# Performance work log

Measured on AMD Instinct MI355X. Metric: run time of the kernel, lower is better.

The kernel has to match this reference:

```python
import jax, jax.numpy as jnp
import numpy as np

SIZE = 7
SIGMA = 1.5
K1 = 0.01
K2 = 0.03
DATA_RANGE = 2.0
NP_ = SIZE * SIZE
COV_NORM = NP_ / (NP_ - 1)
PAD = SIZE // 2


def _gaussian_window(size=SIZE, sigma=SIGMA, channels=1):
    x = np.arange(size) - size // 2
    g = np.exp(-x**2 / (2.0 * sigma**2))[None, :]
    g = (g.T @ g)
    g = g / g.sum()
    w = np.tile(g[None, None], (channels, 1, 1, 1))  # [C,1,size,size]
    return jnp.asarray(w, dtype=jnp.float32)


def _dwconv(x, w):
    # depthwise conv2d, zero padding PAD, stride 1; x: [N,C,H,W], w: [C,1,k,k]
    c = x.shape[1]
    return jax.lax.conv_general_dilated(
        x, w, window_strides=(1, 1), padding=[(PAD, PAD), (PAD, PAD)],
        dimension_numbers=('NCHW', 'OIHW', 'NCHW'), feature_group_count=c)


def setup_inputs() -> dict:
    key = jax.random.key(0)
    k1, k2 = jax.random.split(key)
    X = jax.random.uniform(k1, (64, 1, 320, 320), dtype=jnp.float32)
    Y = jax.random.uniform(k2, (64, 1, 320, 320), dtype=jnp.float32)
    window = _gaussian_window()
    return {"X": X, "Y": Y, "window": window}


def reference(X, Y, window):
    C1 = (K1 * DATA_RANGE) ** 2
    C2 = (K2 * DATA_RANGE) ** 2
    mux = _dwconv(X, window)
    muy = _dwconv(Y, window)
    mux_sq = mux * mux
    muy_sq = muy * muy
    muxy = mux * muy
    sigmax_sq = (_dwconv(X * X, window) - mux_sq) * COV_NORM
    sigmay_sq = (_dwconv(Y * Y, window) - muy_sq) * COV_NORM
    sigmaxy = (_dwconv(X * Y, window) - muxy) * COV_NORM
    ssim_map = ((2 * muxy + C1) * (2 * sigmaxy + C2)) / \
               ((mux_sq + muy_sq + C1) * (sigmax_sq + sigmay_sq + C2))
    return 1.0 - ssim_map.mean()
```

## Files before the change

### kernel.cpp

```cpp
#include <hip/hip_runtime.h>
#include <math.h>


#define TW 64
#define TH 16
#define LW 72
#define LH 22
#define WI 320
#define HI 320
#define NI 64
#define NBLK (5 * 20 * NI)
#define NPIX ((double)NI * WI * HI)

typedef float v4 __attribute__((ext_vector_type(4)));

struct W7 { float w[7]; };

__global__ __launch_bounds__(256) void ssim_kernel(
    const float* __restrict__ X, const float* __restrict__ Y,
    W7 wv, float* __restrict__ partial)
{
    __shared__ __align__(16) float buf[5 * LH * 64];
    __shared__ float wsum[4];

    float* sX = buf;
    float* sY = buf + LH * LW;

    const int tid = threadIdx.x;
    const int tx0 = blockIdx.x * TW;
    const int ty0 = blockIdx.y * TH;
    const int n   = blockIdx.z;
    const float* __restrict__ Xn = X + (size_t)n * (WI * HI);
    const float* __restrict__ Yn = Y + (size_t)n * (WI * HI);

    for (int i = tid; i < LH * LW; i += 256) {
        int r  = i / LW;
        int c  = i - r * LW;
        int gy = ty0 - 3 + r;
        int gx = tx0 - 3 + c;
        float xv = 0.f, yv = 0.f;
        if (c < 70 && (unsigned)gy < (unsigned)HI && (unsigned)gx < (unsigned)WI) {
            int idx = gy * WI + gx;
            xv = Xn[idx];
            yv = Yn[idx];
        }
        sX[i] = xv;
        sY[i] = yv;
    }
    __syncthreads();

    float hreg[2][5][4];
#pragma unroll
    for (int it = 0; it < 2; ++it) {
        int g = tid + it * 256;
        if (g < 352) {
            int r  = g >> 4;
            int c0 = (g & 15) << 2;
            const v4* px = (const v4*)&sX[r * LW + c0];
            const v4* py = (const v4*)&sY[r * LW + c0];
            v4 xa = px[0], xb = px[1], xc = px[2];
            v4 ya = py[0], yb = py[1], yc = py[2];
            float xv[12] = {xa.x,xa.y,xa.z,xa.w, xb.x,xb.y,xb.z,xb.w, xc.x,xc.y,xc.z,xc.w};
            float yv[12] = {ya.x,ya.y,ya.z,ya.w, yb.x,yb.y,yb.z,yb.w, yc.x,yc.y,yc.z,yc.w};
            float xx[12], yy[12], xy[12];
#pragma unroll
            for (int e = 0; e < 12; ++e) {
                xx[e] = xv[e] * xv[e];
                yy[e] = yv[e] * yv[e];
                xy[e] = xv[e] * yv[e];
            }
#pragma unroll
            for (int j = 0; j < 4; ++j) {
                float ax = 0.f, ay = 0.f, axx = 0.f, ayy = 0.f, axy = 0.f;
#pragma unroll
                for (int d = 0; d < 7; ++d) {
                    float w = wv.w[d];
                    ax  += w * xv[j + d];
                    ay  += w * yv[j + d];
                    axx += w * xx[j + d];
                    ayy += w * yy[j + d];
                    axy += w * xy[j + d];
                }
                hreg[it][0][j] = ax;  hreg[it][1][j] = ay;
                hreg[it][2][j] = axx; hreg[it][3][j] = ayy; hreg[it][4][j] = axy;
            }
        }
    }
    __syncthreads();

#pragma unroll
    for (int it = 0; it < 2; ++it) {
        int g = tid + it * 256;
        if (g < 352) {
            int r  = g >> 4;
            int c0 = (g & 15) << 2;
#pragma unroll
            for (int ch = 0; ch < 5; ++ch) {
                v4 t = { hreg[it][ch][0], hreg[it][ch][1],
                         hreg[it][ch][2], hreg[it][ch][3] };
                *(v4*)&buf[ch * (LH * 64) + r * 64 + c0] = t;
            }
        }
    }
    __syncthreads();

    {
        int r  = tid >> 4;
        int c0 = (tid & 15) << 2;
        v4 mx  = {0.f,0.f,0.f,0.f}, my  = {0.f,0.f,0.f,0.f};
        v4 sxx = {0.f,0.f,0.f,0.f}, syy = {0.f,0.f,0.f,0.f}, sxy = {0.f,0.f,0.f,0.f};
#pragma unroll
        for (int d = 0; d < 7; ++d) {
            float w = wv.w[d];
            int off = (r + d) * 64 + c0;
            mx  += w * *(const v4*)&buf[0 * 1408 + off];
            my  += w * *(const v4*)&buf[1 * 1408 + off];
            sxx += w * *(const v4*)&buf[2 * 1408 + off];
            syy += w * *(const v4*)&buf[3 * 1408 + off];
            sxy += w * *(const v4*)&buf[4 * 1408 + off];
        }
        const float C1 = 0.0004f, C2 = 0.0036f, COVN = 49.f / 48.f;
        v4 mxsq = mx * mx;
        v4 mysq = my * my;
        v4 mxy  = mx * my;
        v4 vx   = (sxx - mxsq) * COVN;
        v4 vy   = (syy - mysq) * COVN;
        v4 vxy  = (sxy - mxy)  * COVN;
        v4 num  = (2.f * mxy + C1) * (2.f * vxy + C2);
        v4 den  = (mxsq + mysq + C1) * (vx + vy + C2);
        v4 q;
        q.x = num.x * __builtin_amdgcn_rcpf(den.x);
        q.y = num.y * __builtin_amdgcn_rcpf(den.y);
        q.z = num.z * __builtin_amdgcn_rcpf(den.z);
        q.w = num.w * __builtin_amdgcn_rcpf(den.w);
        float lsum = (q.x + q.y) + (q.z + q.w);

#pragma unroll
        for (int off = 32; off > 0; off >>= 1)
            lsum += __shfl_down(lsum, off, 64);
        if ((tid & 63) == 0) wsum[tid >> 6] = lsum;
        __syncthreads();
        if (tid == 0) {
            int bid = (blockIdx.z * gridDim.y + blockIdx.y) * gridDim.x + blockIdx.x;
            partial[bid] = (wsum[0] + wsum[1]) + (wsum[2] + wsum[3]);
        }
    }
}

__global__ __launch_bounds__(256) void ssim_finalize(
    const float* __restrict__ partial, float* __restrict__ out)
{
    __shared__ double ws[4];
    const int tid = threadIdx.x;
    double s = 0.0;
    for (int i = tid; i < NBLK; i += 256) s += (double)partial[i];
#pragma unroll
    for (int off = 32; off > 0; off >>= 1)
        s += __shfl_down(s, off, 64);
    if ((tid & 63) == 0) ws[tid >> 6] = s;
    __syncthreads();
    if (tid == 0)
        out[0] = (float)(1.0 - ((ws[0] + ws[1]) + (ws[2] + ws[3])) / NPIX);
}

extern "C" void kernel_launch(void* const* d_in, const int* in_sizes, int n_in,
                              void* d_out, int out_size, void* d_ws, size_t ws_size,
                              hipStream_t stream) {
    const float* X = (const float*)d_in[0];
    const float* Y = (const float*)d_in[1];
    W7 wv;
    {
        double g[7], s = 0.0;
        for (int i = 0; i < 7; ++i) {
            double x = (double)(i - 3);
            g[i] = exp(-(x * x) / (2.0 * 1.5 * 1.5));
            s += g[i];
        }
        for (int i = 0; i < 7; ++i) wv.w[i] = (float)(g[i] / s);
    }

    float* partial = (float*)d_ws;

    dim3 grid(WI / TW, HI / TH, NI);
    ssim_kernel<<<grid, 256, 0, stream>>>(X, Y, wv, partial);
    ssim_finalize<<<1, 256, 0, stream>>>(partial, (float*)d_out);
}
```

Measured before the change: 122.1 us.

## Reorder separable SSIM to vertical-first column tasks reading global directly

```diff
diff --git a/kernel.cpp b/kernel.cpp
--- a/kernel.cpp
+++ b/kernel.cpp
@@ -2,148 +2,139 @@
 #include <math.h>
 
 
-#define TW 64
-#define TH 16
-#define LW 72
-#define LH 22
 #define WI 320
 #define HI 320
 #define NI 64
-#define NBLK (5 * 20 * NI)
+#define TW 64
+#define TH 32
+#define GXD 5
+#define GYD 10
+#define NBLK (GXD * GYD * NI)
+#define LSTR 72
 #define NPIX ((double)NI * WI * HI)
 
 typedef float v4 __attribute__((ext_vector_type(4)));
 
 struct W7 { float w[7]; };
 
+template <bool INTERIOR>
+__device__ __forceinline__ void column_task(
+    const float* __restrict__ Xn, const float* __restrict__ Yn,
+    const W7& wv, float* __restrict__ vbuf, int tx0, int ty0, int band, int ci)
+{
+    const int gx  = tx0 + ci - 3;
+    const bool xok = (unsigned)gx < (unsigned)WI;
+    const int gy0 = ty0 + band * 8 - 3;
+
+    float acc[5][8];
+#pragma unroll
+    for (int ch = 0; ch < 5; ++ch)
+#pragma unroll
+        for (int r = 0; r < 8; ++r) acc[ch][r] = 0.f;
+
+#pragma unroll
+    for (int j = 0; j < 14; ++j) {
+        const int gy = gy0 + j;
+        float xv = 0.f, yv = 0.f;
+        const bool ok = INTERIOR ? xok : (xok && ((unsigned)gy < (unsigned)HI));
+        if (ok) {
+            int idx = gy * WI + gx;
+            xv = Xn[idx];
+            yv = Yn[idx];
+        }
+        const float pxx = xv * xv, pyy = yv * yv, pxy = xv * yv;
+#pragma unroll
+        for (int r = 0; r < 8; ++r) {
+            const int d = j - r;
+            if (d >= 0 && d < 7) {
+                const float w = wv.w[d];
+                acc[0][r] += w * xv;
+                acc[1][r] += w * yv;
+                acc[2][r] += w * pxx;
+                acc[3][r] += w * pyy;
+                acc[4][r] += w * pxy;
+            }
+        }
+    }
+#pragma unroll
+    for (int ch = 0; ch < 5; ++ch)
+#pragma unroll
+        for (int r = 0; r < 8; ++r)
+            vbuf[ch * (TH * LSTR) + (band * 8 + r) * LSTR + (ci + 1)] = acc[ch][r];
+}
+
 __global__ __launch_bounds__(256) void ssim_kernel(
     const float* __restrict__ X, const float* __restrict__ Y,
     W7 wv, float* __restrict__ partial)
 {
-    __shared__ __align__(16) float buf[5 * LH * 64];
+    __shared__ __align__(16) float vbuf[5 * TH * LSTR];
     __shared__ float wsum[4];
-
-    float* sX = buf;
-    float* sY = buf + LH * LW;
 
     const int tid = threadIdx.x;
     const int tx0 = blockIdx.x * TW;
     const int ty0 = blockIdx.y * TH;
-    const int n   = blockIdx.z;
-    const float* __restrict__ Xn = X + (size_t)n * (WI * HI);
-    const float* __restrict__ Yn = Y + (size_t)n * (WI * HI);
+    const float* __restrict__ Xn = X + (size_t)blockIdx.z * (WI * HI);
+    const float* __restrict__ Yn = Y + (size_t)blockIdx.z * (WI * HI);
 
-    for (int i = tid; i < LH * LW; i += 256) {
-        int r  = i / LW;
-        int c  = i - r * LW;
-        int gy = ty0 - 3 + r;
-        int gx = tx0 - 3 + c;
-        float xv = 0.f, yv = 0.f;
-        if (c < 70 && (unsigned)gy < (unsigned)HI && (unsigned)gx < (unsigned)WI) {
-            int idx = gy * WI + gx;
-            xv = Xn[idx];
-            yv = Yn[idx];
-        }
-        sX[i] = xv;
-        sY[i] = yv;
+    const bool interior = (blockIdx.y >= 1) && (blockIdx.y <= GYD - 2);
+    if (interior) {
+        column_task<true>(Xn, Yn, wv, vbuf, tx0, ty0, tid >> 6, tid & 63);
+        if (tid < 24) column_task<true>(Xn, Yn, wv, vbuf, tx0, ty0, tid / 6, 64 + tid % 6);
+    } else {
+        column_task<false>(Xn, Yn, wv, vbuf, tx0, ty0, tid >> 6, tid & 63);
+        if (tid < 24) column_task<false>(Xn, Yn, wv, vbuf, tx0, ty0, tid / 6, 64 + tid % 6);
     }
     __syncthreads();
 
-    float hreg[2][5][4];
+    const float C1 = 0.0004f, C2 = 0.0036f, COVN = 49.f / 48.f;
+    const int xg   = (tid & 15) << 2;
+    const int row0 = tid >> 4;
+
+    float lsum = 0.f;
 #pragma unroll
-    for (int it = 0; it < 2; ++it) {
-        int g = tid + it * 256;
-        if (g < 352) {
-            int r  = g >> 4;
-            int c0 = (g & 15) << 2;
-            const v4* px = (const v4*)&sX[r * LW + c0];
-            const v4* py = (const v4*)&sY[r * LW + c0];
-            v4 xa = px[0], xb = px[1], xc = px[2];
-            v4 ya = py[0], yb = py[1], yc = py[2];
-            float xv[12] = {xa.x,xa.y,xa.z,xa.w, xb.x,xb.y,xb.z,xb.w, xc.x,xc.y,xc.z,xc.w};
-            float yv[12] = {ya.x,ya.y,ya.z,ya.w, yb.x,yb.y,yb.z,yb.w, yc.x,yc.y,yc.z,yc.w};
-            float xx[12], yy[12], xy[12];
+    for (int pass = 0; pass < 2; ++pass) {
+        const int row = row0 + pass * 16;
+        float f[5][12];
 #pragma unroll
-            for (int e = 0; e < 12; ++e) {
-                xx[e] = xv[e] * xv[e];
-                yy[e] = yv[e] * yv[e];
-                xy[e] = xv[e] * yv[e];
+        for (int ch = 0; ch < 5; ++ch) {
+            const v4* p = (const v4*)&vbuf[ch * (TH * LSTR) + row * LSTR + xg];
+            v4 a = p[0], b = p[1], c = p[2];
+            f[ch][0] = a.x; f[ch][1] = a.y; f[ch][2]  = a.z; f[ch][3]  = a.w;
+            f[ch][4] = b.x; f[ch][5] = b.y; f[ch][6]  = b.z; f[ch][7]  = b.w;
+            f[ch][8] = c.x; f[ch][9] = c.y; f[ch][10] = c.z; f[ch][11] = c.w;
+        }
+#pragma unroll
+        for (int j = 0; j < 4; ++j) {
+            float mx = 0.f, my = 0.f, sxx = 0.f, syy = 0.f, sxy = 0.f;
+#pragma unroll
+            for (int d = 0; d < 7; ++d) {
+                const float w = wv.w[d];
+                mx  += w * f[0][j + d + 1];
+                my  += w * f[1][j + d + 1];
+                sxx += w * f[2][j + d + 1];
+                syy += w * f[3][j + d + 1];
+                sxy += w * f[4][j + d + 1];
             }
-#pragma unroll
-            for (int j = 0; j < 4; ++j) {
-                float ax = 0.f, ay = 0.f, axx = 0.f, ayy = 0.f, axy = 0.f;
-#pragma unroll
-                for (int d = 0; d < 7; ++d) {
-                    float w = wv.w[d];
-                    ax  += w * xv[j + d];
-                    ay  += w * yv[j + d];
-                    axx += w * xx[j + d];
-                    ayy += w * yy[j + d];
-                    axy += w * xy[j + d];
-                }
-                hreg[it][0][j] = ax;  hreg[it][1][j] = ay;
-                hreg[it][2][j] = axx; hreg[it][3][j] = ayy; hreg[it][4][j] = axy;
-            }
+            const float mxsq = mx * mx;
+            const float mysq = my * my;
+            const float mxy  = mx * my;
+            const float vx   = (sxx - mxsq) * COVN;
+            const float vy   = (syy - mysq) * COVN;
+            const float vxy  = (sxy - mxy)  * COVN;
+            const float num  = (2.f * mxy + C1) * (2.f * vxy + C2);
+            const float den  = (mxsq + mysq + C1) * (vx + vy + C2);
+            lsum += num * __builtin_amdgcn_rcpf(den);
         }
     }
-    __syncthreads();
 
 #pragma unroll
-    for (int it = 0; it < 2; ++it) {
-        int g = tid + it * 256;
-        if (g < 352) {
-            int r  = g >> 4;
-            int c0 = (g & 15) << 2;
-#pragma unroll
-            for (int ch = 0; ch < 5; ++ch) {
-                v4 t = { hreg[it][ch][0], hreg[it][ch][1],
-                         hreg[it][ch][2], hreg[it][ch][3] };
-                *(v4*)&buf[ch * (LH * 64) + r * 64 + c0] = t;
-            }
-        }
-    }
+    for (int off = 32; off > 0; off >>= 1)
+        lsum += __shfl_down(lsum, off, 64);
+    if ((tid & 63) == 0) wsum[tid >> 6] = lsum;
     __syncthreads();
-
-    {
-        int r  = tid >> 4;
-        int c0 = (tid & 15) << 2;
-        v4 mx  = {0.f,0.f,0.f,0.f}, my  = {0.f,0.f,0.f,0.f};
-        v4 sxx = {0.f,0.f,0.f,0.f}, syy = {0.f,0.f,0.f,0.f}, sxy = {0.f,0.f,0.f,0.f};
-#pragma unroll
-        for (int d = 0; d < 7; ++d) {
-            float w = wv.w[d];
-            int off = (r + d) * 64 + c0;
-            mx  += w * *(const v4*)&buf[0 * 1408 + off];
-            my  += w * *(const v4*)&buf[1 * 1408 + off];
-            sxx += w * *(const v4*)&buf[2 * 1408 + off];
-            syy += w * *(const v4*)&buf[3 * 1408 + off];
-            sxy += w * *(const v4*)&buf[4 * 1408 + off];
-        }
-        const float C1 = 0.0004f, C2 = 0.0036f, COVN = 49.f / 48.f;
-        v4 mxsq = mx * mx;
-        v4 mysq = my * my;
-        v4 mxy  = mx * my;
-        v4 vx   = (sxx - mxsq) * COVN;
-        v4 vy   = (syy - mysq) * COVN;
-        v4 vxy  = (sxy - mxy)  * COVN;
-        v4 num  = (2.f * mxy + C1) * (2.f * vxy + C2);
-        v4 den  = (mxsq + mysq + C1) * (vx + vy + C2);
-        v4 q;
-        q.x = num.x * __builtin_amdgcn_rcpf(den.x);
-        q.y = num.y * __builtin_amdgcn_rcpf(den.y);
-        q.z = num.z * __builtin_amdgcn_rcpf(den.z);
-        q.w = num.w * __builtin_amdgcn_rcpf(den.w);
-        float lsum = (q.x + q.y) + (q.z + q.w);
-
-#pragma unroll
-        for (int off = 32; off > 0; off >>= 1)
-            lsum += __shfl_down(lsum, off, 64);
-        if ((tid & 63) == 0) wsum[tid >> 6] = lsum;
-        __syncthreads();
-        if (tid == 0) {
-            int bid = (blockIdx.z * gridDim.y + blockIdx.y) * gridDim.x + blockIdx.x;
-            partial[bid] = (wsum[0] + wsum[1]) + (wsum[2] + wsum[3]);
-        }
+    if (tid == 0) {
+        int bid = (blockIdx.z * GYD + blockIdx.y) * GXD + blockIdx.x;
+        partial[bid] = (wsum[0] + wsum[1]) + (wsum[2] + wsum[3]);
     }
 }
 
@@ -181,7 +172,7 @@
 
     float* partial = (float*)d_ws;
 
-    dim3 grid(WI / TW, HI / TH, NI);
+    dim3 grid(GXD, GYD, NI);
     ssim_kernel<<<grid, 256, 0, stream>>>(X, Y, wv, partial);
     ssim_finalize<<<1, 256, 0, stream>>>(partial, (float*)d_out);
 }
```

After: 114.6 us. -6.2%, faster.
